# Performance work log

Measured on AMD Instinct MI355X. Metric: run time of the kernel, lower is better.

The kernel has to match this reference:

```python
import jax, jax.numpy as jnp
import numpy as np

N_NODES = 50000
IN_C, HID_C, OUT_C = 128, 128, 64
N_EDGES = 600000
DROPOUT_P = 0.5


def setup_inputs() -> dict:
    key = jax.random.key(0)
    k1, k2, k3, k4, k5, k6 = jax.random.split(key, 6)
    x = jax.random.normal(k1, (N_NODES, IN_C), dtype=jnp.float32)
    edge_index = jax.random.randint(k2, (2, N_EDGES), 0, N_NODES, dtype=jnp.int64)
    s1 = 1.0 / np.sqrt(IN_C)
    s2 = 1.0 / np.sqrt(HID_C)
    W1 = jax.random.uniform(k3, (IN_C, HID_C), jnp.float32, -s1, s1)
    b1 = jnp.zeros((HID_C,), jnp.float32)
    W2 = jax.random.uniform(k4, (HID_C, OUT_C), jnp.float32, -s2, s2)
    b2 = jnp.zeros((OUT_C,), jnp.float32)
    return {"x": x, "W1": W1, "b1": b1, "W2": W2, "b2": b2, "edge_index": edge_index}


def reference(x, W1, b1, W2, b2, edge_index):
    N = x.shape[0]
    self_loops = jnp.arange(N, dtype=edge_index.dtype)
    src = jnp.concatenate([edge_index[0], self_loops])  # [E+N]
    dst = jnp.concatenate([edge_index[1], self_loops])
    # symmetric GCN normalization with self-loops (gcn_norm)
    deg = jax.ops.segment_sum(jnp.ones(dst.shape, x.dtype), dst, num_segments=N)
    dinv = jnp.where(deg > 0, jax.lax.rsqrt(deg), 0.0)
    norm = dinv[src] * dinv[dst]  # [E+N]

    def conv(h, W, b):
        h = h @ W  # dense transform first (smaller message dim)
        msg = h[src] * norm[:, None]  # gather + scale, [E+N, C]
        return jax.ops.segment_sum(msg, dst, num_segments=N) + b

    h = jax.nn.relu(conv(x, W1, b1))
    # dropout p=0.5 with fixed key (training mode, deterministic reference)
    keep = jax.random.bernoulli(jax.random.key(42), 1.0 - DROPOUT_P, h.shape)
    h = jnp.where(keep, h / (1.0 - DROPOUT_P), 0.0)
    return conv(h, W2, b2)
```

## Files before the change

### kernel.cpp

```cpp
#include <hip/hip_runtime.h>


#define NN      50000
#define INC     128
#define HIDC    128
#define OUTC    64
#define NE      600000
#define NB      ((NN + 255) / 256)
#define CAP     64

typedef unsigned short bf16_t;
typedef short bf16x8 __attribute__((ext_vector_type(8)));
typedef float f32x4  __attribute__((ext_vector_type(4)));

__device__ __forceinline__ unsigned short f2bf(float f) {
  unsigned u = __float_as_uint(f);
  u += 0x7fffu + ((u >> 16) & 1u);
  return (unsigned short)(u >> 16);
}

__device__ __forceinline__ void tf_round(unsigned &x0, unsigned &x1, int r) {
  x0 += x1;
  x1 = (x1 << r) | (x1 >> (32 - r));
  x1 ^= x0;
}

__device__ __forceinline__ void threefry_0_42(unsigned &x0, unsigned &x1) {
  const unsigned ks0 = 0u, ks1 = 42u, ks2 = 0x1BD11BDAu ^ 42u;
  x0 += ks0; x1 += ks1;
  tf_round(x0,x1,13); tf_round(x0,x1,15); tf_round(x0,x1,26); tf_round(x0,x1, 6);
  x0 += ks1; x1 += ks2 + 1u;
  tf_round(x0,x1,17); tf_round(x0,x1,29); tf_round(x0,x1,16); tf_round(x0,x1,24);
  x0 += ks2; x1 += ks0 + 2u;
  tf_round(x0,x1,13); tf_round(x0,x1,15); tf_round(x0,x1,26); tf_round(x0,x1, 6);
  x0 += ks0; x1 += ks1 + 3u;
  tf_round(x0,x1,17); tf_round(x0,x1,29); tf_round(x0,x1,16); tf_round(x0,x1,24);
  x0 += ks1; x1 += ks2 + 4u;
  tf_round(x0,x1,13); tf_round(x0,x1,15); tf_round(x0,x1,26); tf_round(x0,x1, 6);
  x0 += ks2; x1 += ks0 + 5u;
}

__device__ __forceinline__ bool keep_bit(unsigned idx) {
  unsigned x0 = 0u, x1 = idx;
  threefry_0_42(x0, x1);
  return ((x0 ^ x1) & 0x80000000u) == 0u;
}

__global__ __launch_bounds__(256)
void prep0(const unsigned* __restrict__ ew, int* __restrict__ flag,
           int* __restrict__ cnt) {
  const int b = blockIdx.x, t = threadIdx.x;
  if (b < NB) {
    int idx = b * 256 + t;
    if (idx < NN) cnt[idx] = 0;
  } else {
    __shared__ unsigned acc[256];
    unsigned v = 0;
    for (int i = t; i < 2048; i += 256) v |= ew[2 * i + 1];
    acc[t] = v;
    __syncthreads();
    for (int s = 128; s > 0; s >>= 1) {
      if (t < s) acc[t] |= acc[t + s];
      __syncthreads();
    }
    if (t == 0) *flag = (acc[0] == 0u) ? 1 : 0;
  }
}

__global__ __launch_bounds__(256)
void bucket_direct(const void* __restrict__ ei, const int* __restrict__ flag,
                   int* __restrict__ cnt, int* __restrict__ ssrc) {
  int t = blockIdx.x * 256 + threadIdx.x;
  if (t >= NE) return;
  int s, d;
  if (*flag) {
    s = (int)((const long long*)ei)[t];
    d = (int)((const long long*)ei)[NE + t];
  } else {
    s = ((const int*)ei)[t];
    d = ((const int*)ei)[NE + t];
  }
  int slot = atomicAdd(&cnt[d], 1);
  if (slot < CAP) ssrc[d * CAP + slot] = s;
}

__global__ __launch_bounds__(256)
void calc_dinv(const int* __restrict__ cnt, float* __restrict__ dinv) {
  int t = blockIdx.x * 256 + threadIdx.x;
  if (t < NN) dinv[t] = 1.0f / sqrtf((float)(cnt[t] + 1));
}

template<int C, bool IN_BF16>
__global__ __launch_bounds__(256, 3)
void gemm_mfma(const void* __restrict__ Xv, const float* __restrict__ W,
               const float* __restrict__ dinv, bf16_t* __restrict__ Ab, int n) {
  constexpr int K  = 128;
  constexpr int KS = 136;
  constexpr int CT16 = C / 16;
  __shared__ bf16_t xs[64 * KS];
  __shared__ bf16_t wsT[C * KS];

  const int tid = threadIdx.x;
  const int rb  = blockIdx.x * 64;

  for (int i = tid; i < C * (K / 8); i += 256) {
    int nn = i % C, kc = i / C;
    ushort4 lo, hi;
    lo.x = f2bf(W[(size_t)(kc * 8 + 0) * C + nn]);
    lo.y = f2bf(W[(size_t)(kc * 8 + 1) * C + nn]);
    lo.z = f2bf(W[(size_t)(kc * 8 + 2) * C + nn]);
    lo.w = f2bf(W[(size_t)(kc * 8 + 3) * C + nn]);
    hi.x = f2bf(W[(size_t)(kc * 8 + 4) * C + nn]);
    hi.y = f2bf(W[(size_t)(kc * 8 + 5) * C + nn]);
    hi.z = f2bf(W[(size_t)(kc * 8 + 6) * C + nn]);
    hi.w = f2bf(W[(size_t)(kc * 8 + 7) * C + nn]);
    *(ushort4*)&wsT[nn * KS + kc * 8]     = lo;
    *(ushort4*)&wsT[nn * KS + kc * 8 + 4] = hi;
  }
  for (int i = tid; i < 64 * (K / 4); i += 256) {
    int r = i >> 5, kq = i & 31;
    int row = rb + r;
    ushort4 o = make_ushort4(0, 0, 0, 0);
    if (row < n) {
      if (IN_BF16) {
        o = *(const ushort4*)((const bf16_t*)Xv + (size_t)row * K + kq * 4);
      } else {
        float4 v = *(const float4*)((const float*)Xv + (size_t)row * K + kq * 4);
        o.x = f2bf(v.x); o.y = f2bf(v.y); o.z = f2bf(v.z); o.w = f2bf(v.w);
      }
    }
    *(ushort4*)&xs[r * KS + kq * 4] = o;
  }
  __syncthreads();

  const int wv   = tid >> 6;
  const int lane = tid & 63;
  const int m    = lane & 15;
  const int q    = lane >> 4;

  f32x4 acc[CT16];
#pragma unroll
  for (int c = 0; c < CT16; c++) acc[c] = (f32x4){0.f, 0.f, 0.f, 0.f};

#pragma unroll
  for (int k0 = 0; k0 < K; k0 += 32) {
    bf16x8 a = *(bf16x8*)&xs[(wv * 16 + m) * KS + k0 + q * 8];
#pragma unroll
    for (int c = 0; c < CT16; c++) {
      bf16x8 b = *(bf16x8*)&wsT[(c * 16 + m) * KS + k0 + q * 8];
      acc[c] = __builtin_amdgcn_mfma_f32_16x16x32_bf16(a, b, acc[c], 0, 0, 0);
    }
  }

  const int rowq = rb + wv * 16 + q * 4;
#pragma unroll
  for (int r = 0; r < 4; r++) {
    int row = rowq + r;
    if (row < n) {
      float dv = dinv[row];
#pragma unroll
      for (int c = 0; c < CT16; c++)
        Ab[(size_t)row * C + c * 16 + m] = f2bf(acc[c][r] * dv);
    }
  }
}

__device__ __forceinline__ void acc_u2(float4 &a, uint2 v) {
  a.x += __uint_as_float(v.x << 16);
  a.y += __uint_as_float(v.x & 0xffff0000u);
  a.z += __uint_as_float(v.y << 16);
  a.w += __uint_as_float(v.y & 0xffff0000u);
}

__global__ __launch_bounds__(256)
void agg1(const bf16_t* __restrict__ A1b, const int* __restrict__ cnt,
          const int* __restrict__ ssrc, const float* __restrict__ dinv,
          const float* __restrict__ b1, bf16_t* __restrict__ Hb) {
  int node = (blockIdx.x * 256 + threadIdx.x) >> 5;
  int lane = threadIdx.x & 31;
  if (node >= NN) return;

  const uint2* A4 = (const uint2*)A1b;
  float4 acc = make_float4(0.f, 0.f, 0.f, 0.f);
  acc_u2(acc, A4[(size_t)node * 32 + lane]);
  int e = node * CAP;
  int end = e + min(cnt[node], CAP);
  for (; e + 3 < end; e += 4) {
    int s0 = ssrc[e], s1 = ssrc[e+1], s2 = ssrc[e+2], s3 = ssrc[e+3];
    uint2 v0 = A4[(size_t)s0 * 32 + lane];
    uint2 v1 = A4[(size_t)s1 * 32 + lane];
    uint2 v2 = A4[(size_t)s2 * 32 + lane];
    uint2 v3 = A4[(size_t)s3 * 32 + lane];
    acc_u2(acc, v0); acc_u2(acc, v1); acc_u2(acc, v2); acc_u2(acc, v3);
  }
  for (; e < end; e++)
    acc_u2(acc, A4[(size_t)ssrc[e] * 32 + lane]);

  float dv = dinv[node];
  int col = lane * 4;
  float4 bb = *(const float4*)&b1[col];
  float h0 = fmaxf(acc.x * dv + bb.x, 0.f);
  float h1 = fmaxf(acc.y * dv + bb.y, 0.f);
  float h2 = fmaxf(acc.z * dv + bb.z, 0.f);
  float h3 = fmaxf(acc.w * dv + bb.w, 0.f);
  unsigned base = (unsigned)node * HIDC + (unsigned)col;
  ushort4 o;
  o.x = keep_bit(base)     ? f2bf(2.f * h0) : 0;
  o.y = keep_bit(base + 1) ? f2bf(2.f * h1) : 0;
  o.z = keep_bit(base + 2) ? f2bf(2.f * h2) : 0;
  o.w = keep_bit(base + 3) ? f2bf(2.f * h3) : 0;
  ((ushort4*)Hb)[(size_t)node * 32 + lane] = o;
}

__global__ __launch_bounds__(256)
void agg2(const bf16_t* __restrict__ A2b, const int* __restrict__ cnt,
          const int* __restrict__ ssrc, const float* __restrict__ dinv,
          const float* __restrict__ b2, float* __restrict__ out) {
  int node = (blockIdx.x * 256 + threadIdx.x) >> 4;
  int lane = threadIdx.x & 15;
  if (node >= NN) return;

  const uint2* A4 = (const uint2*)A2b;
  float4 acc = make_float4(0.f, 0.f, 0.f, 0.f);
  acc_u2(acc, A4[(size_t)node * 16 + lane]);
  int e = node * CAP;
  int end = e + min(cnt[node], CAP);
  for (; e + 3 < end; e += 4) {
    int s0 = ssrc[e], s1 = ssrc[e+1], s2 = ssrc[e+2], s3 = ssrc[e+3];
    uint2 v0 = A4[(size_t)s0 * 16 + lane];
    uint2 v1 = A4[(size_t)s1 * 16 + lane];
    uint2 v2 = A4[(size_t)s2 * 16 + lane];
    uint2 v3 = A4[(size_t)s3 * 16 + lane];
    acc_u2(acc, v0); acc_u2(acc, v1); acc_u2(acc, v2); acc_u2(acc, v3);
  }
  for (; e < end; e++)
    acc_u2(acc, A4[(size_t)ssrc[e] * 16 + lane]);

  float dv = dinv[node];
  float4 bb = *(const float4*)&b2[lane * 4];
  ((float4*)out)[(size_t)node * 16 + lane] =
    make_float4(acc.x*dv + bb.x, acc.y*dv + bb.y, acc.z*dv + bb.z, acc.w*dv + bb.w);
}

extern "C" void kernel_launch(void* const* d_in, const int* in_sizes, int n_in,
                              void* d_out, int out_size, void* d_ws, size_t ws_size,
                              hipStream_t stream) {
  const float* x  = (const float*)d_in[0];
  const float* W1 = (const float*)d_in[1];
  const float* b1 = (const float*)d_in[2];
  const float* W2 = (const float*)d_in[3];
  const float* b2 = (const float*)d_in[4];
  const void*  ei = d_in[5];
  float* out = (float*)d_out;

  int*    flag = (int*)d_ws;
  int*    cnt  = flag + 64;
  int*    ssrc = cnt + 50048;
  float*  dinv = (float*)(ssrc + NN * CAP);
  bf16_t* A1b  = (bf16_t*)(dinv + 50048);
  bf16_t* Hb   = A1b + 6400000;
  bf16_t* A2b  = Hb + 6400000;

  prep0<<<NB + 1, 256, 0, stream>>>((const unsigned*)ei, flag, cnt);

  bucket_direct<<<(NE + 255) / 256, 256, 0, stream>>>(ei, flag, cnt, ssrc);
  calc_dinv<<<NB, 256, 0, stream>>>(cnt, dinv);

  const int rtiles = (NN + 63) / 64;

  gemm_mfma<HIDC, false><<<rtiles, 256, 0, stream>>>(x, W1, dinv, A1b, NN);
  agg1<<<(NN * 32 + 255) / 256, 256, 0, stream>>>(A1b, cnt, ssrc, dinv, b1, Hb);

  gemm_mfma<OUTC, true><<<rtiles, 256, 0, stream>>>(Hb, W2, dinv, A2b, NN);
  agg2<<<(NN * 16 + 255) / 256, 256, 0, stream>>>(A2b, cnt, ssrc, dinv, b2, out);
}
```

Before: 195.0 us.

## Fuse edge bucketing with first GEMM and compute degree norm on the fly

Merges the edge-bucketing kernel and the first MFMA GEMM into one launch, with separate block ranges for each, since the GEMM no longer needs dinv. The dinv array and its kernel are removed. The source-side normalization is now applied during layer-1 aggregation by reading cnt[src] and computing rsqrt per edge, while the destination scaling stays in the epilogue. This cuts two launches and a dependency barrier, at the cost of extra random cnt loads and a reciprocal square root per edge in agg1.

```diff
diff --git a/kernel.cpp b/kernel.cpp
--- a/kernel.cpp
+++ b/kernel.cpp
@@ -8,6 +8,8 @@
 #define NE      600000
 #define NB      ((NN + 255) / 256)
 #define CAP     64
+#define EPB     1024
+#define EBB     ((NE + EPB - 1) / EPB)
 
 typedef unsigned short bf16_t;
 typedef short bf16x8 __attribute__((ext_vector_type(8)));
@@ -67,41 +69,37 @@
   }
 }
 
-__global__ __launch_bounds__(256)
-void bucket_direct(const void* __restrict__ ei, const int* __restrict__ flag,
-                   int* __restrict__ cnt, int* __restrict__ ssrc) {
-  int t = blockIdx.x * 256 + threadIdx.x;
-  if (t >= NE) return;
-  int s, d;
-  if (*flag) {
-    s = (int)((const long long*)ei)[t];
-    d = (int)((const long long*)ei)[NE + t];
-  } else {
-    s = ((const int*)ei)[t];
-    d = ((const int*)ei)[NE + t];
-  }
-  int slot = atomicAdd(&cnt[d], 1);
-  if (slot < CAP) ssrc[d * CAP + slot] = s;
-}
-
-__global__ __launch_bounds__(256)
-void calc_dinv(const int* __restrict__ cnt, float* __restrict__ dinv) {
-  int t = blockIdx.x * 256 + threadIdx.x;
-  if (t < NN) dinv[t] = 1.0f / sqrtf((float)(cnt[t] + 1));
-}
-
-template<int C, bool IN_BF16>
 __global__ __launch_bounds__(256, 3)
-void gemm_mfma(const void* __restrict__ Xv, const float* __restrict__ W,
-               const float* __restrict__ dinv, bf16_t* __restrict__ Ab, int n) {
-  constexpr int K  = 128;
-  constexpr int KS = 136;
-  constexpr int CT16 = C / 16;
+void mega1(const void* __restrict__ ei, const int* __restrict__ flag,
+           int* __restrict__ cnt, int* __restrict__ ssrc,
+           const float* __restrict__ X, const float* __restrict__ W,
+           bf16_t* __restrict__ Ab, int n) {
+  constexpr int K  = 128, C = HIDC, KS = 136, CT16 = C / 16;
   __shared__ bf16_t xs[64 * KS];
   __shared__ bf16_t wsT[C * KS];
-
   const int tid = threadIdx.x;
-  const int rb  = blockIdx.x * 64;
+
+  if (blockIdx.x < EBB) {
+    const int base = blockIdx.x * EPB;
+    const int isI64 = *flag;
+    for (int i = tid; i < EPB; i += 256) {
+      int t = base + i;
+      if (t >= NE) break;
+      int s, d;
+      if (isI64) {
+        s = (int)((const long long*)ei)[t];
+        d = (int)((const long long*)ei)[NE + t];
+      } else {
+        s = ((const int*)ei)[t];
+        d = ((const int*)ei)[NE + t];
+      }
+      int slot = atomicAdd(&cnt[d], 1);
+      if (slot < CAP) ssrc[d * CAP + slot] = s;
+    }
+    return;
+  }
+
+  const int rb = (blockIdx.x - EBB) * 64;
 
   for (int i = tid; i < C * (K / 8); i += 256) {
     int nn = i % C, kc = i / C;
@@ -122,21 +120,15 @@
     int row = rb + r;
     ushort4 o = make_ushort4(0, 0, 0, 0);
     if (row < n) {
-      if (IN_BF16) {
-        o = *(const ushort4*)((const bf16_t*)Xv + (size_t)row * K + kq * 4);
-      } else {
-        float4 v = *(const float4*)((const float*)Xv + (size_t)row * K + kq * 4);
-        o.x = f2bf(v.x); o.y = f2bf(v.y); o.z = f2bf(v.z); o.w = f2bf(v.w);
-      }
+      float4 v = *(const float4*)&X[(size_t)row * K + kq * 4];
+      o.x = f2bf(v.x); o.y = f2bf(v.y); o.z = f2bf(v.z); o.w = f2bf(v.w);
     }
     *(ushort4*)&xs[r * KS + kq * 4] = o;
   }
   __syncthreads();
 
-  const int wv   = tid >> 6;
-  const int lane = tid & 63;
-  const int m    = lane & 15;
-  const int q    = lane >> 4;
+  const int wv = tid >> 6, lane = tid & 63;
+  const int m = lane & 15, q = lane >> 4;
 
   f32x4 acc[CT16];
 #pragma unroll
@@ -157,12 +149,18 @@
   for (int r = 0; r < 4; r++) {
     int row = rowq + r;
     if (row < n) {
-      float dv = dinv[row];
 #pragma unroll
       for (int c = 0; c < CT16; c++)
-        Ab[(size_t)row * C + c * 16 + m] = f2bf(acc[c][r] * dv);
-    }
-  }
+        Ab[(size_t)row * C + c * 16 + m] = f2bf(acc[c][r]);
+    }
+  }
+}
+
+__device__ __forceinline__ void acc_u2s(float4 &a, uint2 v, float s) {
+  a.x = fmaf(__uint_as_float(v.x << 16),        s, a.x);
+  a.y = fmaf(__uint_as_float(v.x & 0xffff0000u), s, a.y);
+  a.z = fmaf(__uint_as_float(v.y << 16),        s, a.z);
+  a.w = fmaf(__uint_as_float(v.y & 0xffff0000u), s, a.w);
 }
 
 __device__ __forceinline__ void acc_u2(float4 &a, uint2 v) {
@@ -172,37 +170,47 @@
   a.w += __uint_as_float(v.y & 0xffff0000u);
 }
 
+__device__ __forceinline__ float dinv_of(int c) {
+  return 1.0f / sqrtf((float)(c + 1));
+}
+
 __global__ __launch_bounds__(256)
 void agg1(const bf16_t* __restrict__ A1b, const int* __restrict__ cnt,
-          const int* __restrict__ ssrc, const float* __restrict__ dinv,
-          const float* __restrict__ b1, bf16_t* __restrict__ Hb) {
+          const int* __restrict__ ssrc, const float* __restrict__ b1,
+          bf16_t* __restrict__ Hb) {
   int node = (blockIdx.x * 256 + threadIdx.x) >> 5;
   int lane = threadIdx.x & 31;
   if (node >= NN) return;
 
   const uint2* A4 = (const uint2*)A1b;
+  const int cn = cnt[node];
+  const float dn = dinv_of(cn);
   float4 acc = make_float4(0.f, 0.f, 0.f, 0.f);
-  acc_u2(acc, A4[(size_t)node * 32 + lane]);
+  acc_u2s(acc, A4[(size_t)node * 32 + lane], dn);
   int e = node * CAP;
-  int end = e + min(cnt[node], CAP);
+  int end = e + min(cn, CAP);
   for (; e + 3 < end; e += 4) {
     int s0 = ssrc[e], s1 = ssrc[e+1], s2 = ssrc[e+2], s3 = ssrc[e+3];
+    float d0 = dinv_of(cnt[s0]), d1 = dinv_of(cnt[s1]);
+    float d2 = dinv_of(cnt[s2]), d3 = dinv_of(cnt[s3]);
     uint2 v0 = A4[(size_t)s0 * 32 + lane];
     uint2 v1 = A4[(size_t)s1 * 32 + lane];
     uint2 v2 = A4[(size_t)s2 * 32 + lane];
     uint2 v3 = A4[(size_t)s3 * 32 + lane];
-    acc_u2(acc, v0); acc_u2(acc, v1); acc_u2(acc, v2); acc_u2(acc, v3);
-  }
-  for (; e < end; e++)
-    acc_u2(acc, A4[(size_t)ssrc[e] * 32 + lane]);
-
-  float dv = dinv[node];
+    acc_u2s(acc, v0, d0); acc_u2s(acc, v1, d1);
+    acc_u2s(acc, v2, d2); acc_u2s(acc, v3, d3);
+  }
+  for (; e < end; e++) {
+    int s = ssrc[e];
+    acc_u2s(acc, A4[(size_t)s * 32 + lane], dinv_of(cnt[s]));
+  }
+
   int col = lane * 4;
   float4 bb = *(const float4*)&b1[col];
-  float h0 = fmaxf(acc.x * dv + bb.x, 0.f);
-  float h1 = fmaxf(acc.y * dv + bb.y, 0.f);
-  float h2 = fmaxf(acc.z * dv + bb.z, 0.f);
-  float h3 = fmaxf(acc.w * dv + bb.w, 0.f);
+  float h0 = fmaxf(acc.x * dn + bb.x, 0.f);
+  float h1 = fmaxf(acc.y * dn + bb.y, 0.f);
+  float h2 = fmaxf(acc.z * dn + bb.z, 0.f);
+  float h3 = fmaxf(acc.w * dn + bb.w, 0.f);
   unsigned base = (unsigned)node * HIDC + (unsigned)col;
   ushort4 o;
   o.x = keep_bit(base)     ? f2bf(2.f * h0) : 0;
@@ -212,19 +220,84 @@
   ((ushort4*)Hb)[(size_t)node * 32 + lane] = o;
 }
 
+__global__ __launch_bounds__(256, 3)
+void gemm2(const bf16_t* __restrict__ Hb, const float* __restrict__ W,
+           const int* __restrict__ cnt, bf16_t* __restrict__ Ab, int n) {
+  constexpr int K = 128, C = OUTC, KS = 136, CT16 = C / 16;
+  __shared__ bf16_t xs[64 * KS];
+  __shared__ bf16_t wsT[C * KS];
+  const int tid = threadIdx.x;
+  const int rb  = blockIdx.x * 64;
+
+  for (int i = tid; i < C * (K / 8); i += 256) {
+    int nn = i % C, kc = i / C;
+    ushort4 lo, hi;
+    lo.x = f2bf(W[(size_t)(kc * 8 + 0) * C + nn]);
+    lo.y = f2bf(W[(size_t)(kc * 8 + 1) * C + nn]);
+    lo.z = f2bf(W[(size_t)(kc * 8 + 2) * C + nn]);
+    lo.w = f2bf(W[(size_t)(kc * 8 + 3) * C + nn]);
+    hi.x = f2bf(W[(size_t)(kc * 8 + 4) * C + nn]);
+    hi.y = f2bf(W[(size_t)(kc * 8 + 5) * C + nn]);
+    hi.z = f2bf(W[(size_t)(kc * 8 + 6) * C + nn]);
+    hi.w = f2bf(W[(size_t)(kc * 8 + 7) * C + nn]);
+    *(ushort4*)&wsT[nn * KS + kc * 8]     = lo;
+    *(ushort4*)&wsT[nn * KS + kc * 8 + 4] = hi;
+  }
+  for (int i = tid; i < 64 * (K / 8); i += 256) {
+    int r = i >> 4, kc = i & 15;
+    int row = rb + r;
+    uint4 o = make_uint4(0, 0, 0, 0);
+    if (row < n)
+      o = *(const uint4*)(Hb + (size_t)row * K + kc * 8);
+    *(uint4*)&xs[r * KS + kc * 8] = o;
+  }
+  __syncthreads();
+
+  const int wv = tid >> 6, lane = tid & 63;
+  const int m = lane & 15, q = lane >> 4;
+
+  f32x4 acc[CT16];
+#pragma unroll
+  for (int c = 0; c < CT16; c++) acc[c] = (f32x4){0.f, 0.f, 0.f, 0.f};
+
+#pragma unroll
+  for (int k0 = 0; k0 < K; k0 += 32) {
+    bf16x8 a = *(bf16x8*)&xs[(wv * 16 + m) * KS + k0 + q * 8];
+#pragma unroll
+    for (int c = 0; c < CT16; c++) {
+      bf16x8 b = *(bf16x8*)&wsT[(c * 16 + m) * KS + k0 + q * 8];
+      acc[c] = __builtin_amdgcn_mfma_f32_16x16x32_bf16(a, b, acc[c], 0, 0, 0);
+    }
+  }
+
+  const int rowq = rb + wv * 16 + q * 4;
+#pragma unroll
+  for (int r = 0; r < 4; r++) {
+    int row = rowq + r;
+    if (row < n) {
+      float dv = dinv_of(cnt[row]);
+#pragma unroll
+      for (int c = 0; c < CT16; c++)
+        Ab[(size_t)row * C + c * 16 + m] = f2bf(acc[c][r] * dv);
+    }
+  }
+}
+
 __global__ __launch_bounds__(256)
 void agg2(const bf16_t* __restrict__ A2b, const int* __restrict__ cnt,
-          const int* __restrict__ ssrc, const float* __restrict__ dinv,
-          const float* __restrict__ b2, float* __restrict__ out) {
+          const int* __restrict__ ssrc, const float* __restrict__ b2,
+          float* __restrict__ out) {
   int node = (blockIdx.x * 256 + threadIdx.x) >> 4;
   int lane = threadIdx.x & 15;
   if (node >= NN) return;
 
   const uint2* A4 = (const uint2*)A2b;
+  const int cn = cnt[node];
+  const float dn = dinv_of(cn);
   float4 acc = make_float4(0.f, 0.f, 0.f, 0.f);
   acc_u2(acc, A4[(size_t)node * 16 + lane]);
   int e = node * CAP;
-  int end = e + min(cnt[node], CAP);
+  int end = e + min(cn, CAP);
   for (; e + 3 < end; e += 4) {
     int s0 = ssrc[e], s1 = ssrc[e+1], s2 = ssrc[e+2], s3 = ssrc[e+3];
     uint2 v0 = A4[(size_t)s0 * 16 + lane];
@@ -236,10 +309,9 @@
   for (; e < end; e++)
     acc_u2(acc, A4[(size_t)ssrc[e] * 16 + lane]);
 
-  float dv = dinv[node];
   float4 bb = *(const float4*)&b2[lane * 4];
   ((float4*)out)[(size_t)node * 16 + lane] =
-    make_float4(acc.x*dv + bb.x, acc.y*dv + bb.y, acc.z*dv + bb.z, acc.w*dv + bb.w);
+    make_float4(acc.x*dn + bb.x, acc.y*dn + bb.y, acc.z*dn + bb.z, acc.w*dn + bb.w);
 }
 
 extern "C" void kernel_launch(void* const* d_in, const int* in_sizes, int n_in,
@@ -256,21 +328,18 @@
   int*    flag = (int*)d_ws;
   int*    cnt  = flag + 64;
   int*    ssrc = cnt + 50048;
-  float*  dinv = (float*)(ssrc + NN * CAP);
-  bf16_t* A1b  = (bf16_t*)(dinv + 50048);
+  bf16_t* A1b  = (bf16_t*)(ssrc + NN * CAP);
   bf16_t* Hb   = A1b + 6400000;
   bf16_t* A2b  = Hb + 6400000;
 
+  const int rtiles = (NN + 63) / 64;
+
   prep0<<<NB + 1, 256, 0, stream>>>((const unsigned*)ei, flag, cnt);
 
-  bucket_direct<<<(NE + 255) / 256, 256, 0, stream>>>(ei, flag, cnt, ssrc);
-  calc_dinv<<<NB, 256, 0, stream>>>(cnt, dinv);
-
-  const int rtiles = (NN + 63) / 64;
-
-  gemm_mfma<HIDC, false><<<rtiles, 256, 0, stream>>>(x, W1, dinv, A1b, NN);
-  agg1<<<(NN * 32 + 255) / 256, 256, 0, stream>>>(A1b, cnt, ssrc, dinv, b1, Hb);
-
-  gemm_mfma<OUTC, true><<<rtiles, 256, 0, stream>>>(Hb, W2, dinv, A2b, NN);
-  agg2<<<(NN * 16 + 255) / 256, 256, 0, stream>>>(A2b, cnt, ssrc, dinv, b2, out);
-}
+  mega1<<<EBB + rtiles, 256, 0, stream>>>(ei, flag, cnt, ssrc, x, W1, A1b, NN);
+
+  agg1<<<(NN * 32 + 255) / 256, 256, 0, stream>>>(A1b, cnt, ssrc, b1, Hb);
+
+  gemm2<<<rtiles, 256, 0, stream>>>(Hb, W2, cnt, A2b, NN);
+  agg2<<<(NN * 16 + 255) / 256, 256, 0, stream>>>(A2b, cnt, ssrc, b2, out);
+}
```

New measurement: 205.0 us. 5.2% more time.
